# Kernel tuning notes

Measured on AMD Instinct MI355X. Metric: run time of the kernel, lower is better.

The kernel has to match this reference:

```python
import jax, jax.numpy as jnp
import numpy as np

DIM = 128
NUM_HEADS = 4
HEAD_DIM = DIM // NUM_HEADS
KSIZE = 7
DILATION = 1
SCALE = HEAD_DIM ** -0.5


def _rpb_bias(rpb):
    # Faithful to _get_rpb_indices: indices do NOT depend on query position.
    coords = np.stack(np.meshgrid(np.arange(KSIZE), np.arange(KSIZE), indexing='ij'))
    coords = coords.reshape(2, -1).T  # [K*K, 2]
    rel = coords - KSIZE // 2 + (KSIZE - 1)
    return rpb[:, rel[:, 0], rel[:, 1]]  # [NH, K*K]


def setup_inputs() -> dict:
    key = jax.random.key(0)
    ks = jax.random.split(key, 6)
    B, H, W = 4, 56, 56
    x = jax.random.normal(ks[0], (B, H, W, DIM), dtype=jnp.float32)
    qkv_w = jax.random.normal(ks[1], (3 * DIM, DIM), dtype=jnp.float32) * 0.02
    qkv_b = jnp.zeros((3 * DIM,), dtype=jnp.float32)
    rpb = jax.random.normal(ks[2], (NUM_HEADS, 2 * KSIZE - 1, 2 * KSIZE - 1), dtype=jnp.float32) * 0.02
    proj_w = jax.random.normal(ks[3], (DIM, DIM), dtype=jnp.float32) * 0.02
    proj_b = jnp.zeros((DIM,), dtype=jnp.float32)
    return {"x": x, "qkv_w": qkv_w, "qkv_b": qkv_b, "rpb": rpb, "proj_w": proj_w, "proj_b": proj_b}


def reference(x, qkv_w, qkv_b, rpb, proj_w, proj_b):
    B, H, W, C = x.shape
    qkv = x @ qkv_w.T + qkv_b                                   # [B,H,W,3C]
    qkv = qkv.reshape(B, H, W, 3, NUM_HEADS, HEAD_DIM).transpose(3, 0, 4, 1, 2, 5)
    q, k, v = qkv[0], qkv[1], qkv[2]                            # [B,NH,H,W,HD]

    pad = (KSIZE // 2) * DILATION
    # Zero padding — padded positions stay in the softmax (faithful, no masking).
    kp = jnp.pad(k, ((0, 0), (0, 0), (pad, pad), (pad, pad), (0, 0)))
    vp = jnp.pad(v, ((0, 0), (0, 0), (pad, pad), (pad, pad), (0, 0)))

    off = jnp.arange(0, KSIZE * DILATION, DILATION)
    idx_i = jnp.arange(H)[:, None] + off[None, :]               # [H,K]
    idx_j = jnp.arange(W)[:, None] + off[None, :]               # [W,K]
    Ai = idx_i[:, None, :, None]                                # [H,1,K,1]
    Aj = idx_j[None, :, None, :]                                # [1,W,1,K]
    k_win = kp[:, :, Ai, Aj, :].reshape(B, NUM_HEADS, H, W, KSIZE * KSIZE, HEAD_DIM)
    v_win = vp[:, :, Ai, Aj, :].reshape(B, NUM_HEADS, H, W, KSIZE * KSIZE, HEAD_DIM)

    bias = _rpb_bias(rpb)                                       # [NH, K*K]
    attn = jnp.einsum('bnhwd,bnhwkd->bnhwk', q, k_win) * SCALE
    attn = attn + bias[None, :, None, None, :]
    attn = jax.nn.softmax(attn, axis=-1)
    out = jnp.einsum('bnhwk,bnhwkd->bnhwd', attn, v_win)        # [B,NH,H,W,HD]
    out = out.transpose(0, 2, 3, 1, 4).reshape(B, H, W, C)
    return out @ proj_w.T + proj_b
```

## Files before the change

### kernel.cpp

```cpp
#include <hip/hip_runtime.h>

#define NPIX   3136
#define MROWS  12544
#define QKV_STRIDE 1605632
#define SCALE  0.17677669529663687f
#define KVS    136
#define HP     140

typedef __attribute__((ext_vector_type(8))) _Float16 half8;
typedef __attribute__((ext_vector_type(2))) _Float16 v2h;
typedef __attribute__((ext_vector_type(4))) float    f32x4;

#if defined(__has_builtin)
#if __has_builtin(__builtin_amdgcn_fdot2)
#define HAS_FDOT2 1
#endif
#endif

__device__ __forceinline__ float quad_reduce_sum(float x) {
    x += __int_as_float(__builtin_amdgcn_mov_dpp(__float_as_int(x), 0xB1, 0xF, 0xF, true));
    x += __int_as_float(__builtin_amdgcn_mov_dpp(__float_as_int(x), 0x4E, 0xF, 0xF, true));
    return x;
}

__device__ __forceinline__ float dot8h(half8 a, half8 b, float acc) {
#ifdef HAS_FDOT2
    union { half8 v; v2h p[4]; } ua, ub;
    ua.v = a; ub.v = b;
    acc = __builtin_amdgcn_fdot2(ua.p[0], ub.p[0], acc, false);
    acc = __builtin_amdgcn_fdot2(ua.p[1], ub.p[1], acc, false);
    acc = __builtin_amdgcn_fdot2(ua.p[2], ub.p[2], acc, false);
    acc = __builtin_amdgcn_fdot2(ua.p[3], ub.p[3], acc, false);
#else
#pragma unroll
    for (int i = 0; i < 8; ++i) acc += (float)a[i] * (float)b[i];
#endif
    return acc;
}

template<int BM, int BN, int WM, int WN>
__global__ __launch_bounds__(256)
void qkv_mfma(const float* __restrict__ A, const float* __restrict__ W,
              const float* __restrict__ bias, _Float16* __restrict__ outh,
              const float* __restrict__ pw, _Float16* __restrict__ pwh)
{
    constexpr int WTM = BM / WM;
    constexpr int WTN = BN / WN;
    constexpr int FM  = WTM / 16;
    constexpr int FN  = WTN / 16;
    constexpr int AIT = BM * 16 / 256;
    constexpr int WIT = BN * 16 / 256;
    const int t  = threadIdx.x;
    const int f  = blockIdx.x;

    if (f < 16) {
        int idx = f * 256 + t;
        float4 v = *reinterpret_cast<const float4*>(pw + (size_t)idx * 4);
        union { _Float16 h[4]; uint2 u; } cv;
        cv.h[0] = (_Float16)v.x; cv.h[1] = (_Float16)v.y;
        cv.h[2] = (_Float16)v.z; cv.h[3] = (_Float16)v.w;
        *reinterpret_cast<uint2*>(pwh + (size_t)idx * 4) = cv.u;
    }

    const int g    = f & 7;
    const int w_   = f >> 3;
    const int xi   = w_ / 3;
    const int yc   = w_ % 3;
    const int xhat = (g & 1) ? 25 + xi : xi;
    if (xhat >= ((g & 1) ? 49 : 25)) return;
    const int row0 = ((g >> 1) * 49 + xhat) * BM;
    const int col0 = yc * BN;

    const int w  = t >> 6;
    const int l  = t & 63;
    const int wm = w / WN;
    const int wn = w % WN;

    __shared__ _Float16 Ah[BM * 128];
    __shared__ _Float16 Wh[BN * 128];

    float4 pa[AIT], pwr[WIT];

#pragma unroll
    for (int it = 0; it < AIT; ++it) {
        int idx = t + it * 256;
        int r = idx >> 4, k0 = (idx & 15) << 2;
        pa[it] = *reinterpret_cast<const float4*>(A + (size_t)(row0 + r) * 128 + k0);
    }
#pragma unroll
    for (int it = 0; it < WIT; ++it) {
        int idx = t + it * 256;
        int r = idx >> 4, k0 = (idx & 15) << 2;
        pwr[it] = *reinterpret_cast<const float4*>(W + (size_t)(col0 + r) * 128 + k0);
    }
#pragma unroll
    for (int it = 0; it < AIT; ++it) {
        int idx = t + it * 256;
        int r = idx >> 4, k0 = (idx & 15) << 2;
        union { _Float16 h[4]; uint2 u; } cv;
        cv.h[0] = (_Float16)pa[it].x; cv.h[1] = (_Float16)pa[it].y;
        cv.h[2] = (_Float16)pa[it].z; cv.h[3] = (_Float16)pa[it].w;
        *reinterpret_cast<uint2*>(&Ah[r * 128 + (k0 ^ ((r & 7) << 3))]) = cv.u;
    }
#pragma unroll
    for (int it = 0; it < WIT; ++it) {
        int idx = t + it * 256;
        int r = idx >> 4, k0 = (idx & 15) << 2;
        union { _Float16 h[4]; uint2 u; } cv;
        cv.h[0] = (_Float16)pwr[it].x; cv.h[1] = (_Float16)pwr[it].y;
        cv.h[2] = (_Float16)pwr[it].z; cv.h[3] = (_Float16)pwr[it].w;
        *reinterpret_cast<uint2*>(&Wh[r * 128 + (k0 ^ ((r & 7) << 3))]) = cv.u;
    }
    __syncthreads();

#pragma unroll
    for (int it = 0; it < AIT; ++it) {
        int idx = t + it * 256;
        int r = idx >> 4, k0 = 64 + ((idx & 15) << 2);
        pa[it] = *reinterpret_cast<const float4*>(A + (size_t)(row0 + r) * 128 + k0);
    }
#pragma unroll
    for (int it = 0; it < WIT; ++it) {
        int idx = t + it * 256;
        int r = idx >> 4, k0 = 64 + ((idx & 15) << 2);
        pwr[it] = *reinterpret_cast<const float4*>(W + (size_t)(col0 + r) * 128 + k0);
    }

    f32x4 acc[FM][FN];
#pragma unroll
    for (int mf = 0; mf < FM; ++mf)
#pragma unroll
        for (int nf = 0; nf < FN; ++nf) acc[mf][nf] = (f32x4){0.f, 0.f, 0.f, 0.f};

#pragma unroll
    for (int ks = 0; ks < 2; ++ks) {
        const int kb = ks * 32 + ((l >> 4) << 3);
        half8 a[FM], b[FN];
#pragma unroll
        for (int mf = 0; mf < FM; ++mf) {
            int m = wm * WTM + mf * 16 + (l & 15);
            a[mf] = *reinterpret_cast<const half8*>(&Ah[m * 128 + (kb ^ ((m & 7) << 3))]);
        }
#pragma unroll
        for (int nf = 0; nf < FN; ++nf) {
            int n = wn * WTN + nf * 16 + (l & 15);
            b[nf] = *reinterpret_cast<const half8*>(&Wh[n * 128 + (kb ^ ((n & 7) << 3))]);
        }
#pragma unroll
        for (int mf = 0; mf < FM; ++mf)
#pragma unroll
            for (int nf = 0; nf < FN; ++nf)
                acc[mf][nf] = __builtin_amdgcn_mfma_f32_16x16x32_f16(
                    a[mf], b[nf], acc[mf][nf], 0, 0, 0);
    }

#pragma unroll
    for (int it = 0; it < AIT; ++it) {
        int idx = t + it * 256;
        int r = idx >> 4, k0 = 64 + ((idx & 15) << 2);
        union { _Float16 h[4]; uint2 u; } cv;
        cv.h[0] = (_Float16)pa[it].x; cv.h[1] = (_Float16)pa[it].y;
        cv.h[2] = (_Float16)pa[it].z; cv.h[3] = (_Float16)pa[it].w;
        *reinterpret_cast<uint2*>(&Ah[r * 128 + (k0 ^ ((r & 7) << 3))]) = cv.u;
    }
#pragma unroll
    for (int it = 0; it < WIT; ++it) {
        int idx = t + it * 256;
        int r = idx >> 4, k0 = 64 + ((idx & 15) << 2);
        union { _Float16 h[4]; uint2 u; } cv;
        cv.h[0] = (_Float16)pwr[it].x; cv.h[1] = (_Float16)pwr[it].y;
        cv.h[2] = (_Float16)pwr[it].z; cv.h[3] = (_Float16)pwr[it].w;
        *reinterpret_cast<uint2*>(&Wh[r * 128 + (k0 ^ ((r & 7) << 3))]) = cv.u;
    }
    __syncthreads();

#pragma unroll
    for (int ks = 2; ks < 4; ++ks) {
        const int kb = ks * 32 + ((l >> 4) << 3);
        half8 a[FM], b[FN];
#pragma unroll
        for (int mf = 0; mf < FM; ++mf) {
            int m = wm * WTM + mf * 16 + (l & 15);
            a[mf] = *reinterpret_cast<const half8*>(&Ah[m * 128 + (kb ^ ((m & 7) << 3))]);
        }
#pragma unroll
        for (int nf = 0; nf < FN; ++nf) {
            int n = wn * WTN + nf * 16 + (l & 15);
            b[nf] = *reinterpret_cast<const half8*>(&Wh[n * 128 + (kb ^ ((n & 7) << 3))]);
        }
#pragma unroll
        for (int mf = 0; mf < FM; ++mf)
#pragma unroll
            for (int nf = 0; nf < FN; ++nf)
                acc[mf][nf] = __builtin_amdgcn_mfma_f32_16x16x32_f16(
                    a[mf], b[nf], acc[mf][nf], 0, 0, 0);
    }

#pragma unroll
    for (int mf = 0; mf < FM; ++mf) {
#pragma unroll
        for (int nf = 0; nf < FN; ++nf) {
#pragma unroll
            for (int r = 0; r < 4; ++r) {
                int row = row0 + wm * WTM + mf * 16 + ((l >> 4) << 2) + r;
                int col = col0 + wn * WTN + nf * 16 + (l & 15);
                float val = acc[mf][nf][r] + bias[col];
                int b_  = row / NPIX;
                int pix = row - b_ * NPIX;
                int which = col >> 7;
                outh[(size_t)which * QKV_STRIDE +
                     ((size_t)b_ * NPIX + pix) * 128 + (col & 127)] = (_Float16)val;
            }
        }
    }
}

__global__ __launch_bounds__(512, 4)
void natten_proj_k(const _Float16* __restrict__ qb, const _Float16* __restrict__ kb,
                   const _Float16* __restrict__ vb, const float* __restrict__ rpb,
                   const _Float16* __restrict__ pwh, const float* __restrict__ pb,
                   float* __restrict__ out)
{
    extern __shared__ _Float16 smem[];
    _Float16* ksm  = smem;
    _Float16* vsm  = smem + HP * KVS;
    _Float16* atts = smem;

    const int flat = blockIdx.x;
    const int rank = (flat & 7) * 49 + (flat >> 3);
    const int tile = rank % 98;
    const int b    = rank / 98;
    const int ti = (tile / 14) * 8;
    const int tj = (tile % 14) * 4;
    const int t   = threadIdx.x;
    const int sub = t & 3;
    const int px  = (t >> 2) & 31;
    const int pi  = px >> 2;
    const int pj  = px & 3;
    const int h   = t >> 7;

    const _Float16* kbase = kb + (size_t)b * NPIX * 128;
    const _Float16* vbase = vb + (size_t)b * NPIX * 128;

    const int pix = (ti + pi) * 56 + (tj + pj);
    half8 qv = *reinterpret_cast<const half8*>(
        qb + ((size_t)b * NPIX + pix) * 128 + h * 32 + sub * 8);

    for (int e = t; e < HP * 16; e += 512) {
        int p = e >> 4, g = e & 15;
        int wi = p / 10, wj = p - wi * 10;
        int gi = ti - 3 + wi, gj = tj - 3 + wj;
        bool ok = ((unsigned)gi < 56u) && ((unsigned)gj < 56u);
        size_t src = ((size_t)(gi * 56 + gj)) * 128 + g * 8;
        half8 kv = (half8){0,0,0,0,0,0,0,0};
        if (ok) kv = *reinterpret_cast<const half8*>(kbase + src);
        *reinterpret_cast<half8*>(&ksm[p * KVS + g * 8]) = kv;
        half8 vv = (half8){0,0,0,0,0,0,0,0};
        if (ok) vv = *reinterpret_cast<const half8*>(vbase + src);
        *reinterpret_cast<half8*>(&vsm[p * KVS + g * 8]) = vv;
    }

    __syncthreads();

    const float* bias = rpb + h * 169;
    float logits[49];
    float m = -1e30f;
#pragma unroll
    for (int ki = 0; ki < 7; ++ki) {
#pragma unroll
        for (int kj = 0; kj < 7; ++kj) {
            int nb = (pi + ki) * 10 + (pj + kj);
            half8 kk = *reinterpret_cast<const half8*>(&ksm[nb * KVS + h * 32 + sub * 8]);
            float s = dot8h(qv, kk, 0.f);
            s = quad_reduce_sum(s);
            float lg = s * SCALE + bias[(ki + 3) * 13 + (kj + 3)];
            logits[ki * 7 + kj] = lg;
            m = fmaxf(m, lg);
        }
    }

    __syncthreads();

    float sum = 0.f;
#pragma unroll
    for (int n = 0; n < 49; ++n) {
        float e = __expf(logits[n] - m);
        logits[n] = e;
        sum += e;
    }
    float inv = 1.f / sum;

    float o[8] = {0.f, 0.f, 0.f, 0.f, 0.f, 0.f, 0.f, 0.f};
#pragma unroll
    for (int ki = 0; ki < 7; ++ki) {
#pragma unroll
        for (int kj = 0; kj < 7; ++kj) {
            int nb = (pi + ki) * 10 + (pj + kj);
            half8 vv = *reinterpret_cast<const half8*>(&vsm[nb * KVS + h * 32 + sub * 8]);
            float wgt = logits[ki * 7 + kj];
#pragma unroll
            for (int i = 0; i < 8; ++i)
                o[i] += wgt * (float)vv[i];
        }
    }

    const int l   = t & 63;
    const int wv  = t >> 6;
    const int wm  = wv & 1;
    const int wn  = wv >> 1;
    const int kb0 = (l >> 4) << 3;
    half8 wreg[8];
#pragma unroll
    for (int ks = 0; ks < 4; ++ks) {
        const _Float16* wp = pwh + (size_t)(wn * 32 + (l & 15)) * 128 + ks * 32 + kb0;
        wreg[ks]     = *reinterpret_cast<const half8*>(wp);
        wreg[4 + ks] = *reinterpret_cast<const half8*>(wp + 16 * 128);
    }

    {
        half8 r;
#pragma unroll
        for (int i = 0; i < 8; ++i) r[i] = (_Float16)(o[i] * inv);
        *reinterpret_cast<half8*>(&atts[px * KVS + h * 32 + sub * 8]) = r;
    }

    __syncthreads();

    f32x4 acc0 = (f32x4){0.f, 0.f, 0.f, 0.f};
    f32x4 acc1 = (f32x4){0.f, 0.f, 0.f, 0.f};
#pragma unroll
    for (int ks = 0; ks < 4; ++ks) {
        const int kb = ks * 32 + kb0;
        half8 a = *reinterpret_cast<const half8*>(&atts[(wm * 16 + (l & 15)) * KVS + kb]);
        acc0 = __builtin_amdgcn_mfma_f32_16x16x32_f16(a, wreg[ks],     acc0, 0, 0, 0);
        acc1 = __builtin_amdgcn_mfma_f32_16x16x32_f16(a, wreg[4 + ks], acc1, 0, 0, 0);
    }

#pragma unroll
    for (int r = 0; r < 4; ++r) {
        int prow = wm * 16 + ((l >> 4) << 2) + r;
        int gpix = (ti + (prow >> 2)) * 56 + tj + (prow & 3);
        float* dst = out + ((size_t)b * NPIX + gpix) * 128;
        int c0 = wn * 32 + (l & 15);
        dst[c0]      = acc0[r] + pb[c0];
        dst[c0 + 16] = acc1[r] + pb[c0 + 16];
    }
}

extern "C" void kernel_launch(void* const* d_in, const int* in_sizes, int n_in,
                              void* d_out, int out_size, void* d_ws, size_t ws_size,
                              hipStream_t stream)
{
    const float* x      = (const float*)d_in[0];
    const float* qkv_w  = (const float*)d_in[1];
    const float* qkv_b  = (const float*)d_in[2];
    const float* rpb    = (const float*)d_in[3];
    const float* proj_w = (const float*)d_in[4];
    const float* proj_b = (const float*)d_in[5];
    float* out = (float*)d_out;

    _Float16* qbuf = (_Float16*)d_ws;
    _Float16* kbuf = qbuf + (size_t)QKV_STRIDE;
    _Float16* vbuf = kbuf + (size_t)QKV_STRIDE;
    _Float16* pwh  = vbuf + (size_t)QKV_STRIDE;

    hipFuncSetAttribute((const void*)natten_proj_k,
                        hipFuncAttributeMaxDynamicSharedMemorySize,
                        2 * HP * KVS * (int)sizeof(_Float16));

    qkv_mfma<64, 128, 2, 2><<<dim3(600), dim3(256), 0, stream>>>(
        x, qkv_w, qkv_b, qbuf, proj_w, pwh);

    natten_proj_k<<<dim3(392), dim3(512),
                    2 * HP * KVS * sizeof(_Float16), stream>>>(
        qbuf, kbuf, vbuf, rpb, pwh, proj_b, out);
}
```

Measured before the change: 26.87 us.

## Pre-pad K/V in global memory and stage halo via direct global-to-LDS loads

New measurement: 38.16 us. 1.42x slower.

```diff
diff --git a/kernel.cpp b/kernel.cpp
--- a/kernel.cpp
+++ b/kernel.cpp
@@ -1,15 +1,34 @@
 #include <hip/hip_runtime.h>
+#include <stdint.h>
 
 #define NPIX   3136
 #define MROWS  12544
-#define QKV_STRIDE 1605632
 #define SCALE  0.17677669529663687f
-#define KVS    136
+#define ASTR   136
 #define HP     140
+#define HCH    35
+
+#define Q_OFF   0u
+#define Q_SZ    1605632u
+#define PADB    3844u
+#define PAD_BST 492032u
+#define PAD_SZ  1968128u
+#define KP_OFF  (Q_OFF + Q_SZ)
+#define VP_OFF  (KP_OFF + PAD_SZ)
+#define PW_OFF  (VP_OFF + PAD_SZ)
+
+#define KVIDX(p, d) (((p) << 7) + ((d) ^ (((p) & 7) << 3)))
 
 typedef __attribute__((ext_vector_type(8))) _Float16 half8;
 typedef __attribute__((ext_vector_type(2))) _Float16 v2h;
 typedef __attribute__((ext_vector_type(4))) float    f32x4;
+
+typedef __attribute__((address_space(3))) void*       as3_void_ptr;
+typedef const __attribute__((address_space(1))) void* as1_cvoid_ptr;
+
+__device__ __forceinline__ void gld_lds16(const void* g, void* l) {
+    __builtin_amdgcn_global_load_lds((as1_cvoid_ptr)g, (as3_void_ptr)l, 16, 0, 0);
+}
 
 #if defined(__has_builtin)
 #if __has_builtin(__builtin_amdgcn_fdot2)
@@ -41,7 +60,8 @@
 template<int BM, int BN, int WM, int WN>
 __global__ __launch_bounds__(256)
 void qkv_mfma(const float* __restrict__ A, const float* __restrict__ W,
-              const float* __restrict__ bias, _Float16* __restrict__ outh,
+              const float* __restrict__ bias, _Float16* __restrict__ qout,
+              _Float16* __restrict__ kpad, _Float16* __restrict__ vpad,
               const float* __restrict__ pw, _Float16* __restrict__ pwh)
 {
     constexpr int WTM = BM / WM;
@@ -62,6 +82,24 @@
         *reinterpret_cast<uint2*>(pwh + (size_t)idx * 4) = cv.u;
     }
 
+    if (f < 354) {
+        int idx = f * 256 + t;
+        int g   = idx & 15;
+        int r2  = idx >> 4;
+        int pp  = r2 % 708;
+        int q2  = r2 / 708;
+        int bz  = q2 & 3;
+        _Float16* dstb = (q2 >> 2) ? vpad : kpad;
+        int pr, pc;
+        if (pp < 186)      { pr = pp / 62; pc = pp - pr * 62; }
+        else if (pp < 372) { int j = pp - 186; int jr = j / 62; pr = 59 + jr; pc = j - jr * 62; }
+        else               { int j = pp - 372; int jr = j / 6;  pr = 3 + jr;
+                             int c6 = j - jr * 6; pc = (c6 < 3) ? c6 : c6 + 56; }
+        *reinterpret_cast<half8*>(
+            &dstb[((size_t)bz * PADB + pr * 62 + pc) * 128 + g * 8]) =
+            (half8){0,0,0,0,0,0,0,0};
+    }
+
     const int g    = f & 7;
     const int w_   = f >> 3;
     const int xi   = w_ / 3;
@@ -208,22 +246,29 @@
                 int b_  = row / NPIX;
                 int pix = row - b_ * NPIX;
                 int which = col >> 7;
-                outh[(size_t)which * QKV_STRIDE +
-                     ((size_t)b_ * NPIX + pix) * 128 + (col & 127)] = (_Float16)val;
+                _Float16 hv = (_Float16)val;
+                if (which == 0) {
+                    qout[((size_t)b_ * NPIX + pix) * 128 + (col & 127)] = hv;
+                } else {
+                    int rr = pix / 56, cc = pix - rr * 56;
+                    size_t off = ((size_t)b_ * PADB + (rr + 3) * 62 + (cc + 3)) * 128
+                               + (col & 127);
+                    (which == 1 ? kpad : vpad)[off] = hv;
+                }
             }
         }
     }
 }
 
 __global__ __launch_bounds__(512, 4)
-void natten_proj_k(const _Float16* __restrict__ qb, const _Float16* __restrict__ kb,
-                   const _Float16* __restrict__ vb, const float* __restrict__ rpb,
+void natten_proj_k(const _Float16* __restrict__ qb, const _Float16* __restrict__ kpad,
+                   const _Float16* __restrict__ vpad, const float* __restrict__ rpb,
                    const _Float16* __restrict__ pwh, const float* __restrict__ pb,
                    float* __restrict__ out)
 {
     extern __shared__ _Float16 smem[];
     _Float16* ksm  = smem;
-    _Float16* vsm  = smem + HP * KVS;
+    _Float16* vsm  = smem + HP * 128;
     _Float16* atts = smem;
 
     const int flat = blockIdx.x;
@@ -239,30 +284,31 @@
     const int pj  = px & 3;
     const int h   = t >> 7;
 
-    const _Float16* kbase = kb + (size_t)b * NPIX * 128;
-    const _Float16* vbase = vb + (size_t)b * NPIX * 128;
+    const _Float16* kb_ = kpad + (size_t)b * PAD_BST;
+    const _Float16* vb_ = vpad + (size_t)b * PAD_BST;
 
     const int pix = (ti + pi) * 56 + (tj + pj);
     half8 qv = *reinterpret_cast<const half8*>(
         qb + ((size_t)b * NPIX + pix) * 128 + h * 32 + sub * 8);
 
-    for (int e = t; e < HP * 16; e += 512) {
-        int p = e >> 4, g = e & 15;
-        int wi = p / 10, wj = p - wi * 10;
-        int gi = ti - 3 + wi, gj = tj - 3 + wj;
-        bool ok = ((unsigned)gi < 56u) && ((unsigned)gj < 56u);
-        size_t src = ((size_t)(gi * 56 + gj)) * 128 + g * 8;
-        half8 kv = (half8){0,0,0,0,0,0,0,0};
-        if (ok) kv = *reinterpret_cast<const half8*>(kbase + src);
-        *reinterpret_cast<half8*>(&ksm[p * KVS + g * 8]) = kv;
-        half8 vv = (half8){0,0,0,0,0,0,0,0};
-        if (ok) vv = *reinterpret_cast<const half8*>(vbase + src);
-        *reinterpret_cast<half8*>(&vsm[p * KVS + g * 8]) = vv;
+    {
+        const int wv8  = t >> 6;
+        const int lane = t & 63;
+        for (int c = wv8; c < HCH; c += 8) {
+            int e = c * 64 + lane;
+            int p = e >> 4;
+            int g = (e & 15) ^ (p & 7);
+            int wi = p / 10, wj = p - wi * 10;
+            size_t src = ((size_t)((ti + wi) * 62 + (tj + wj))) * 128 + g * 8;
+            gld_lds16(kb_ + src, ksm + (size_t)c * 512);
+            gld_lds16(vb_ + src, vsm + (size_t)c * 512);
+        }
     }
 
     __syncthreads();
 
     const float* bias = rpb + h * 169;
+    const int dl = h * 32 + sub * 8;
     float logits[49];
     float m = -1e30f;
 #pragma unroll
@@ -270,7 +316,7 @@
 #pragma unroll
         for (int kj = 0; kj < 7; ++kj) {
             int nb = (pi + ki) * 10 + (pj + kj);
-            half8 kk = *reinterpret_cast<const half8*>(&ksm[nb * KVS + h * 32 + sub * 8]);
+            half8 kk = *reinterpret_cast<const half8*>(&ksm[KVIDX(nb, dl)]);
             float s = dot8h(qv, kk, 0.f);
             s = quad_reduce_sum(s);
             float lg = s * SCALE + bias[(ki + 3) * 13 + (kj + 3)];
@@ -296,7 +342,7 @@
 #pragma unroll
         for (int kj = 0; kj < 7; ++kj) {
             int nb = (pi + ki) * 10 + (pj + kj);
-            half8 vv = *reinterpret_cast<const half8*>(&vsm[nb * KVS + h * 32 + sub * 8]);
+            half8 vv = *reinterpret_cast<const half8*>(&vsm[KVIDX(nb, dl)]);
             float wgt = logits[ki * 7 + kj];
 #pragma unroll
             for (int i = 0; i < 8; ++i)
@@ -321,7 +367,7 @@
         half8 r;
 #pragma unroll
         for (int i = 0; i < 8; ++i) r[i] = (_Float16)(o[i] * inv);
-        *reinterpret_cast<half8*>(&atts[px * KVS + h * 32 + sub * 8]) = r;
+        *reinterpret_cast<half8*>(&atts[px * ASTR + dl]) = r;
     }
 
     __syncthreads();
@@ -331,7 +377,7 @@
 #pragma unroll
     for (int ks = 0; ks < 4; ++ks) {
         const int kb = ks * 32 + kb0;
-        half8 a = *reinterpret_cast<const half8*>(&atts[(wm * 16 + (l & 15)) * KVS + kb]);
+        half8 a = *reinterpret_cast<const half8*>(&atts[(wm * 16 + (l & 15)) * ASTR + kb]);
         acc0 = __builtin_amdgcn_mfma_f32_16x16x32_f16(a, wreg[ks],     acc0, 0, 0, 0);
         acc1 = __builtin_amdgcn_mfma_f32_16x16x32_f16(a, wreg[4 + ks], acc1, 0, 0, 0);
     }
@@ -359,19 +405,20 @@
     const float* proj_b = (const float*)d_in[5];
     float* out = (float*)d_out;
 
-    _Float16* qbuf = (_Float16*)d_ws;
-    _Float16* kbuf = qbuf + (size_t)QKV_STRIDE;
-    _Float16* vbuf = kbuf + (size_t)QKV_STRIDE;
-    _Float16* pwh  = vbuf + (size_t)QKV_STRIDE;
+    _Float16* wsbase = (_Float16*)d_ws;
+    _Float16* qbuf = wsbase + Q_OFF;
+    _Float16* kpad = wsbase + KP_OFF;
+    _Float16* vpad = wsbase + VP_OFF;
+    _Float16* pwh  = wsbase + PW_OFF;
 
     hipFuncSetAttribute((const void*)natten_proj_k,
                         hipFuncAttributeMaxDynamicSharedMemorySize,
-                        2 * HP * KVS * (int)sizeof(_Float16));
+                        2 * HP * 128 * (int)sizeof(_Float16));
 
     qkv_mfma<64, 128, 2, 2><<<dim3(600), dim3(256), 0, stream>>>(
-        x, qkv_w, qkv_b, qbuf, proj_w, pwh);
+        x, qkv_w, qkv_b, qbuf, kpad, vpad, proj_w, pwh);
 
     natten_proj_k<<<dim3(392), dim3(512),
-                    2 * HP * KVS * sizeof(_Float16), stream>>>(
-        qbuf, kbuf, vbuf, rpb, pwh, proj_b, out);
-}
+                    2 * HP * 128 * sizeof(_Float16), stream>>>(
+        qbuf, kpad, vpad, rpb, pwh, proj_b, out);
+}
```
